# Kernel tuning notes

Measured on AMD Instinct MI355X. Metric: run time of the kernel, lower is better.

Reference implementation:

```python
import jax, jax.numpy as jnp
import numpy as np

SIDE = 64; EMB = 16; CH = 64; K = 64; V = 64; L = 8
N = SIDE * SIDE

def _pos_table(side, d):
    pe = np.array([[p / np.power(10000, 2 * (j // 2) / d) for j in range(d)]
                   if p != 0 else np.zeros(d) for p in range(side)])
    pe[1:, 0::2] = np.sin(pe[1:, 0::2])
    pe[1:, 1::2] = np.cos(pe[1:, 1::2])
    return pe.astype(np.float32)  # [side, d]

def _pos_emb():
    # Replicates torch .view(1, emb, side, 1): plain reshape of [side, emb] -> [emb, side]
    t = _pos_table(SIDE, EMB).reshape(EMB, SIDE)
    xe = np.broadcast_to(t[:, :, None], (EMB, SIDE, SIDE))
    ye = np.broadcast_to(t[:, None, :], (EMB, SIDE, SIDE))
    return jnp.asarray(np.concatenate([xe, ye], 0).reshape(1, 2 * EMB, N))

def _conv_mask():
    # CausalConv mask, see_center=False, 5x5: zero center pixel onward in center row, and all rows below
    m = np.ones((CH, 3, 5, 5), np.float32)
    m[:, :, 2, 2:] = 0.0
    m[:, :, 3:, :] = 0.0
    return jnp.asarray(m)

def _lrelu(x):
    return jnp.where(x >= 0, x, 0.01 * x)  # LeakyReLU(0.01)

def _bn(x, g, b, eps=1e-5):
    # training-mode batch norm (biased variance), channel axis = 1
    axes = (0,) + tuple(range(2, x.ndim))
    m = jnp.mean(x, axes, keepdims=True)
    var = jnp.mean((x - m) ** 2, axes, keepdims=True)
    sh = (1, -1) + (1,) * (x.ndim - 2)
    return g.reshape(sh) * (x - m) / jnp.sqrt(var + eps) + b.reshape(sh)

def _cv1(w, b, x):
    # 1x1 Conv1d: [O,I] x [B,I,N] -> [B,O,N]
    return jnp.einsum('oi,bin->bon', w, x) + b[:, None]

def reference(x, conv_w, conv_b, bn0_g, bn0_b, q_w, q_b, fk_w, fk_b, ck_w, ck_b,
              fv_w, fv_b, cv_w, cv_b, bn_g, bn_b, out_w, out_b):
    B = x.shape[0]
    pos = jnp.broadcast_to(_pos_emb(), (B, 2 * EMB, N))
    mask = jnp.tril(jnp.ones((N, N), jnp.float32))

    # masked causal conv input layer + BN + LeakyReLU
    w = conv_w * _conv_mask()
    h = jax.lax.conv_general_dilated(x, w, (1, 1), [(2, 2), (2, 2)],
                                     dimension_numbers=('NCHW', 'OIHW', 'NCHW'))
    h = h + conv_b[None, :, None, None]
    h = _lrelu(_bn(h, bn0_g, bn0_b)).reshape(B, CH, N)

    k0 = jnp.zeros((B, K, N), x.dtype)
    v0 = jnp.zeros((B, V, N), x.dtype)
    inv_sqrt_k = 1.0 / jnp.sqrt(jnp.float32(K))

    def layer(carry, p):
        h, k, v = carry
        qw, qb, fkw, fkb, ckw, ckb, fvw, fvb, cvw, cvb, g, bb = p
        x0 = jnp.concatenate([h, pos], 1)            # [B, CH+32, N]
        x0k = jnp.concatenate([x0, k], 1)            # [B, 160, N]
        x0v = jnp.concatenate([x0, v], 1)
        fk = jax.nn.sigmoid(_cv1(fkw, fkb, x0k))
        ck = _lrelu(_cv1(ckw, ckb, x0k))
        k_new = fk * k + ck                          # highway-gated persistent K
        fv = jax.nn.sigmoid(_cv1(fvw, fvb, x0v))
        cv_ = _lrelu(_cv1(cvw, cvb, x0v))
        v_new = fv * v + cv_
        q = _lrelu(_cv1(qw, qb, x0))                 # [B, K, N]
        attn = jnp.einsum('bkn,bkm->bnm', q, k) * inv_sqrt_k  # uses OLD k
        attn = attn * mask + (1.0 - mask) * (-10000.0)
        attn = jax.nn.softmax(attn, axis=-1) * mask
        out1 = jnp.einsum('bnm,bvm->bvn', attn, v)   # uses OLD v; [B, V, N]
        # original code computes fc(out1) but discards it (out2 overwritten)
        h2 = _lrelu(_bn(out1, g, bb))
        return (h2, k_new, v_new), None

    params = (q_w, q_b, fk_w, fk_b, ck_w, ck_b, fv_w, fv_b, cv_w, cv_b, bn_g, bn_b)
    (h, k, v), _ = jax.lax.scan(layer, (h, k0, v0), params)

    out = jnp.einsum('oi,bin->bon', out_w, h) + out_b[None, :, None]
    return out.reshape(B, out_w.shape[0], SIDE, SIDE)

def setup_inputs() -> dict:
    key = jax.random.key(0)
    ks = jax.random.split(key, 12)
    s = 0.05
    return {
        'x': jax.random.normal(ks[0], (2, 3, 64, 64), jnp.float32),
        'conv_w': jax.random.normal(ks[1], (CH, 3, 5, 5), jnp.float32) * s,
        'conv_b': jnp.zeros((CH,), jnp.float32),
        'bn0_g': jnp.ones((CH,), jnp.float32),
        'bn0_b': jnp.zeros((CH,), jnp.float32),
        'q_w': jax.random.normal(ks[2], (L, K, CH + 2 * EMB), jnp.float32) * s,
        'q_b': jnp.zeros((L, K), jnp.float32),
        'fk_w': jax.random.normal(ks[3], (L, K, CH + K + 2 * EMB), jnp.float32) * s,
        'fk_b': jnp.zeros((L, K), jnp.float32),
        'ck_w': jax.random.normal(ks[4], (L, K, CH + K + 2 * EMB), jnp.float32) * s,
        'ck_b': jnp.zeros((L, K), jnp.float32),
        'fv_w': jax.random.normal(ks[5], (L, V, CH + V + 2 * EMB), jnp.float32) * s,
        'fv_b': jnp.zeros((L, V), jnp.float32),
        'cv_w': jax.random.normal(ks[6], (L, V, CH + V + 2 * EMB), jnp.float32) * s,
        'cv_b': jnp.zeros((L, V), jnp.float32),
        'bn_g': jnp.ones((L, CH), jnp.float32),
        'bn_b': jnp.zeros((L, CH), jnp.float32),
        'out_w': jax.random.normal(ks[7], (100, V), jnp.float32) * s,
        'out_b': jnp.zeros((100,), jnp.float32),
    }
```

## Files before the change

### kernel.cpp

```cpp
#include <hip/hip_runtime.h>

#define NPIX 4096
#define CHN  64

typedef __attribute__((ext_vector_type(8))) short short8;
typedef __attribute__((ext_vector_type(8))) unsigned short ushort8;
typedef __attribute__((ext_vector_type(4))) unsigned short ushort4v;
typedef __attribute__((ext_vector_type(4))) float f32x4;
typedef __attribute__((ext_vector_type(16))) float f32x16;

__device__ __forceinline__ float lrelu_(float x){ return x >= 0.f ? x : 0.01f*x; }

__device__ __forceinline__ unsigned short f2bf(float x){
  union { float f; unsigned u; } v; v.f = x;
  unsigned r = v.u + 0x7FFF + ((v.u >> 16) & 1);
  return (unsigned short)(r >> 16);
}
__device__ __forceinline__ float bf2f(unsigned short h){
  union { unsigned u; float f; } v; v.u = ((unsigned)h) << 16;
  return v.f;
}
__device__ __forceinline__ float asf_(unsigned u){
  union { unsigned u; float f; } v; v.u = u; return v.f;
}

__global__ void pos_kernel(float* __restrict__ pos){
  int idx = blockIdx.x*256 + threadIdx.x;
  int c = idx >> 12;
  int n = idx & (NPIX-1);
  int bcoord = (c < 16) ? (n >> 6) : (n & 63);
  int a = (c < 16) ? c : (c - 16);
  int flat = a*64 + bcoord;
  int p = flat >> 4;
  int j = flat & 15;
  float val = 0.f;
  if (p != 0){
    float ex = (float)(j & ~1) * (1.f/16.f);
    float w = powf(10000.f, -ex);
    float ang = (float)p * w;
    val = (j & 1) ? cosf(ang) : sinf(ang);
  }
  pos[idx] = val;
}

__global__ void wtr_kernel(const float* __restrict__ qw, const float* __restrict__ fkw,
                           const float* __restrict__ ckw, const float* __restrict__ fvw,
                           const float* __restrict__ cvw, const float* __restrict__ convw,
                           float* __restrict__ wt){
  int idx = blockIdx.x*256 + threadIdx.x;
  if (idx >= 381632) return;
  if (idx < 49152){
    int l = idx / 6144, r = idx % 6144, i = r >> 6, o = r & 63;
    wt[idx] = qw[(l*64 + o)*96 + i];
  } else if (idx < 376832){
    int e = idx - 49152;
    int mat = e / 81920, r = e % 81920;
    int l = r / 10240, rr = r % 10240, i = rr >> 6, o = rr & 63;
    const float* src = (mat==0) ? fkw : (mat==1) ? ckw : (mat==2) ? fvw : cvw;
    wt[idx] = src[(l*64 + o)*160 + i];
  } else {
    int e = idx - 376832;
    int o = e & 63, tap = e >> 6;
    int ci = tap / 25, r = tap % 25;
    wt[idx] = convw[(o*3 + ci)*25 + r];
  }
}

__global__ __launch_bounds__(256) void conv_in_kernel(const float* __restrict__ x,
                                                      const float* __restrict__ cwt,
                                                      const float* __restrict__ cb,
                                                      float* __restrict__ out){
  int t = threadIdx.x;
  int o = t & 63;
  int sub = t >> 6;
  int bid = blockIdx.x;
  int b = bid >> 10;
  int n = ((bid & 1023) << 2) + sub;
  int y = n >> 6, xx = n & 63;
  float acc = cb[o];
  #pragma unroll
  for (int ci=0; ci<3; ++ci){
    const float* xp = x + ((b*3+ci)<<12);
    #pragma unroll
    for (int ky=0; ky<3; ++ky){
      int yy = y + ky - 2;
      if (yy < 0) continue;
      int nk = (ky==2) ? 2 : 5;
      #pragma unroll
      for (int kx=0; kx<5; ++kx){
        if (kx >= nk) break;
        int xc = xx + kx - 2;
        if (xc < 0 || xc > 63) continue;
        acc += xp[(yy<<6) + xc] * cwt[(ci*25 + ky*5 + kx)*64 + o];
      }
    }
  }
  out[(b*CHN+o)*NPIX + n] = acc;
}

__global__ __launch_bounds__(1024) void bn_stats_kernel(const float* __restrict__ xin,
                                                        float* __restrict__ stats){
  int c = blockIdx.x;
  int t = threadIdx.x;
  float s = 0.f, ss = 0.f;
  #pragma unroll
  for (int it=0; it<8; ++it){
    int idx = t + it*1024;
    float v = xin[(((idx>>12))*CHN + c)*NPIX + (idx & (NPIX-1))];
    s += v; ss += v*v;
  }
  #pragma unroll
  for (int o=1; o<64; o<<=1){ s += __shfl_xor(s,o); ss += __shfl_xor(ss,o); }
  __shared__ float ps[16], pq[16];
  if ((t & 63) == 0){ ps[t>>6] = s; pq[t>>6] = ss; }
  __syncthreads();
  if (t == 0){
    float S=0.f, Q=0.f;
    #pragma unroll
    for (int i=0;i<16;++i){ S += ps[i]; Q += pq[i]; }
    float mu = S*(1.f/8192.f);
    float var = Q*(1.f/8192.f) - mu*mu;
    var = fmaxf(var, 0.f);
    stats[c*2]   = mu;
    stats[c*2+1] = rsqrtf(var + 1e-5f);
  }
}

__global__ void bn_apply_kernel(const float* __restrict__ xin, const float* __restrict__ stats,
                                const float* __restrict__ g, const float* __restrict__ bb,
                                float* __restrict__ hout){
  int idx = blockIdx.x*256 + threadIdx.x;
  int e = idx << 2;
  int c = (e >> 12) & 63;
  float mu = stats[c*2], rstd = stats[c*2+1];
  float gain = g[c]*rstd;
  float beta = bb[c] - gain*mu;
  float4 v = *(const float4*)(xin + e);
  float4 r;
  r.x = lrelu_(gain*v.x + beta);
  r.y = lrelu_(gain*v.y + beta);
  r.z = lrelu_(gain*v.z + beta);
  r.w = lrelu_(gain*v.w + beta);
  *(float4*)(hout + e) = r;
}

__global__ __launch_bounds__(256) void bn_apply2_kernel(float* __restrict__ hbuf,
                                                        const float* __restrict__ psum,
                                                        const float* __restrict__ psq,
                                                        const float* __restrict__ g,
                                                        const float* __restrict__ bb){
  int bid = blockIdx.x;
  int ebase = bid << 10;
  int c = (ebase >> 12) & 63;
  int t = threadIdx.x;
  float s = psum[c*256 + t];
  float q = psq[c*256 + t];
  #pragma unroll
  for (int o=1; o<64; o<<=1){ s += __shfl_xor(s,o); q += __shfl_xor(q,o); }
  __shared__ float as[4], aq[4];
  if ((t & 63) == 0){ as[t>>6] = s; aq[t>>6] = q; }
  __syncthreads();
  float S = as[0]+as[1]+as[2]+as[3];
  float Q = aq[0]+aq[1]+aq[2]+aq[3];
  float mu = S*(1.f/8192.f);
  float var = fmaxf(Q*(1.f/8192.f) - mu*mu, 0.f);
  float rstd = rsqrtf(var + 1e-5f);
  float gain = g[c]*rstd;
  float beta = bb[c] - gain*mu;
  float4 v = *(const float4*)(hbuf + ebase + t*4);
  float4 r;
  r.x = lrelu_(gain*v.x + beta);
  r.y = lrelu_(gain*v.y + beta);
  r.z = lrelu_(gain*v.z + beta);
  r.w = lrelu_(gain*v.w + beta);
  *(float4*)(hbuf + ebase + t*4) = r;
}

__global__ __launch_bounds__(256) void cv1_kernel(
    const float* __restrict__ hbuf, const float* __restrict__ pos,
    const float* __restrict__ kold, const float* __restrict__ vold,
    const float* __restrict__ qwt,
    const float* __restrict__ fkwt, const float* __restrict__ ckwt,
    const float* __restrict__ fvwt, const float* __restrict__ cvwt,
    const float* __restrict__ qbi,  const float* __restrict__ fkb,
    const float* __restrict__ ckb,  const float* __restrict__ fvb,
    const float* __restrict__ cvb,
    unsigned short* __restrict__ qh, unsigned short* __restrict__ ql,
    float* __restrict__ knew, unsigned short* __restrict__ khn, unsigned short* __restrict__ kln,
    float* __restrict__ vnew, unsigned short* __restrict__ vhTn, unsigned short* __restrict__ vlTn)
{
  int t = threadIdx.x;
  int o  = t & 63;
  int wv = t >> 6;
  int b    = blockIdx.x >> 8;
  int tile = blockIdx.x & 255;
  int n0 = tile*16 + wv*4;

  const float* hb = hbuf + b*CHN*NPIX + n0;
  const float* kb = kold + b*CHN*NPIX + n0;
  const float* vb = vold + b*CHN*NPIX + n0;
  const float* pb = pos + n0;

  auto load4 = [&](const float* p, float* dst){
    float4 a = *(const float4*)p;
    dst[0]=a.x; dst[1]=a.y; dst[2]=a.z; dst[3]=a.w;
  };

  float x[4];
  long obase = (long)(b*CHN+o)*NPIX + n0;
  size_t nbase = ((size_t)b*NPIX + n0)*64 + o;

  {
    float aq[4];
    float bias = qbi[o];
    #pragma unroll
    for (int j=0;j<4;++j) aq[j]=bias;
    #pragma unroll 4
    for (int i=0;i<64;++i){
      load4(hb + i*NPIX, x);
      float w = qwt[i*64 + o];
      #pragma unroll
      for (int j=0;j<4;++j) aq[j] += w*x[j];
    }
    #pragma unroll 4
    for (int i=0;i<32;++i){
      load4(pb + i*NPIX, x);
      float w = qwt[(64+i)*64 + o];
      #pragma unroll
      for (int j=0;j<4;++j) aq[j] += w*x[j];
    }
    #pragma unroll
    for (int j=0;j<4;++j){
      float v = lrelu_(aq[j]) * 0.125f;
      unsigned short hb16 = f2bf(v);
      qh[nbase + (size_t)j*64] = hb16;
      ql[nbase + (size_t)j*64] = f2bf(v - bf2f(hb16));
    }
  }

  {
    float af[4], ac[4];
    float bf = fkb[o], bc = ckb[o];
    #pragma unroll
    for (int j=0;j<4;++j){ af[j]=bf; ac[j]=bc; }
    #pragma unroll 4
    for (int i=0;i<64;++i){
      load4(hb + i*NPIX, x);
      float wf = fkwt[i*64+o], wc = ckwt[i*64+o];
      #pragma unroll
      for (int j=0;j<4;++j){ af[j] += wf*x[j]; ac[j] += wc*x[j]; }
    }
    #pragma unroll 4
    for (int i=0;i<32;++i){
      load4(pb + i*NPIX, x);
      float wf = fkwt[(64+i)*64+o], wc = ckwt[(64+i)*64+o];
      #pragma unroll
      for (int j=0;j<4;++j){ af[j] += wf*x[j]; ac[j] += wc*x[j]; }
    }
    #pragma unroll 4
    for (int i=0;i<64;++i){
      load4(kb + i*NPIX, x);
      float wf = fkwt[(96+i)*64+o], wc = ckwt[(96+i)*64+o];
      #pragma unroll
      for (int j=0;j<4;++j){ af[j] += wf*x[j]; ac[j] += wc*x[j]; }
    }
    float kv[4];
    load4(kb + o*NPIX, kv);
    #pragma unroll
    for (int j=0;j<4;++j){
      float fk = 1.f/(1.f+__expf(-af[j]));
      float kn = fk*kv[j] + lrelu_(ac[j]);
      knew[obase+j] = kn;
      unsigned short hb16 = f2bf(kn);
      khn[nbase + (size_t)j*64] = hb16;
      kln[nbase + (size_t)j*64] = f2bf(kn - bf2f(hb16));
    }
  }

  {
    float af[4], ac[4];
    float bf = fvb[o], bc = cvb[o];
    #pragma unroll
    for (int j=0;j<4;++j){ af[j]=bf; ac[j]=bc; }
    #pragma unroll 4
    for (int i=0;i<64;++i){
      load4(hb + i*NPIX, x);
      float wf = fvwt[i*64+o], wc = cvwt[i*64+o];
      #pragma unroll
      for (int j=0;j<4;++j){ af[j] += wf*x[j]; ac[j] += wc*x[j]; }
    }
    #pragma unroll 4
    for (int i=0;i<32;++i){
      load4(pb + i*NPIX, x);
      float wf = fvwt[(64+i)*64+o], wc = cvwt[(64+i)*64+o];
      #pragma unroll
      for (int j=0;j<4;++j){ af[j] += wf*x[j]; ac[j] += wc*x[j]; }
    }
    #pragma unroll 4
    for (int i=0;i<64;++i){
      load4(vb + i*NPIX, x);
      float wf = fvwt[(96+i)*64+o], wc = cvwt[(96+i)*64+o];
      #pragma unroll
      for (int j=0;j<4;++j){ af[j] += wf*x[j]; ac[j] += wc*x[j]; }
    }
    float vv[4];
    load4(vb + o*NPIX, vv);
    ushort4v vph, vpl;
    #pragma unroll
    for (int j=0;j<4;++j){
      float fv = 1.f/(1.f+__expf(-af[j]));
      float vn = fv*vv[j] + lrelu_(ac[j]);
      vnew[obase+j] = vn;
      unsigned short hb16 = f2bf(vn);
      vph[j] = hb16;
      vpl[j] = f2bf(vn - bf2f(hb16));
    }
    *(ushort4v*)(vhTn + ((size_t)(b*CHN+o))*NPIX + n0) = vph;
    *(ushort4v*)(vlTn + ((size_t)(b*CHN+o))*NPIX + n0) = vpl;
  }
}

__global__ __launch_bounds__(256) void attn_mfma(
    const unsigned short* __restrict__ qhg, const unsigned short* __restrict__ qlg,
    const unsigned short* __restrict__ khg, const unsigned short* __restrict__ klg,
    const unsigned short* __restrict__ vhg, const unsigned short* __restrict__ vlg,
    float* __restrict__ part)
{
  int bid = 287 - (int)blockIdx.x;
  int b = 0, id = bid;
  if (id >= 144){ b = 1; id -= 144; }
  int pidx = bid;
  int rem = id, k = 0;
  while (rem >= 4*(k+1)){ rem -= 4*(k+1); ++k; }
  int rtg   = 4*k + rem/(k+1);
  int chunk = rem - (rem/(k+1))*(k+1);

  int C0  = chunk << 9;
  int end = min(C0 + 512, rtg*128 + 128);
  int nt  = (end - C0 + 63) >> 6;

  int t = threadIdx.x;
  int w = t >> 6;
  int l = t & 63;
  int q = l & 31;
  int hi = l >> 5;
  int qbase = rtg*128 + w*32;
  int n_g = qbase + q;
  int nmax_w = qbase + 31;

  __shared__ __align__(16) char KH[8192], KL[8192];
  __shared__ __align__(16) char VH[8192], VL[8192];
  __shared__ __align__(16) char PH[4][4096], PL[4][4096];

  const unsigned short* qhp = qhg + (size_t)b*NPIX*64;
  const unsigned short* qlp = qlg + (size_t)b*NPIX*64;
  const unsigned short* khp = khg + (size_t)b*NPIX*64;
  const unsigned short* klp = klg + (size_t)b*NPIX*64;
  const unsigned short* vhp = vhg + (size_t)b*CHN*NPIX;
  const unsigned short* vlp = vlg + (size_t)b*CHN*NPIX;

  short8 qhf[4], qlf[4];
  #pragma unroll
  for (int kc=0; kc<4; ++kc){
    qhf[kc] = *(const short8*)(qhp + (size_t)n_g*64 + kc*16 + hi*8);
    qlf[kc] = *(const short8*)(qlp + (size_t)n_g*64 + kc*16 + hi*8);
  }

  int srow[2], scc8[2], soff[2];
  #pragma unroll
  for (int p=0; p<2; ++p){
    int slot = t + (p<<8);
    int row = slot >> 3, cc = slot & 7;
    srow[p] = row; scc8[p] = cc*8;
    soff[p] = row*128 + ((cc ^ (row & 7)) << 4);
  }
  ushort8 rkh[2], rkl[2], rvh[2], rvl[2];
  auto issue = [&](int m0){
    #pragma unroll
    for (int p=0; p<2; ++p){
      rkh[p] = *(const ushort8*)(khp + (size_t)(m0+srow[p])*64 + scc8[p]);
      rkl[p] = *(const ushort8*)(klp + (size_t)(m0+srow[p])*64 + scc8[p]);
      rvh[p] = *(const ushort8*)(vhp + (size_t)srow[p]*NPIX + m0 + scc8[p]);
      rvl[p] = *(const ushort8*)(vlp + (size_t)srow[p]*NPIX + m0 + scc8[p]);
    }
  };

  f32x16 oacc0, oacc1;
  #pragma unroll
  for (int i=0; i<16; ++i){ oacc0[i]=0.f; oacc1[i]=0.f; }
  float m_run = -1e30f, l_run = 0.f;

  char* phw = PH[w];
  char* plw = PL[w];

  issue(C0);
  for (int ti=0; ti<nt; ++ti){
    int m0 = C0 + (ti<<6);
    __syncthreads();
    #pragma unroll
    for (int p=0; p<2; ++p){
      *(ushort8*)(KH + soff[p]) = rkh[p];
      *(ushort8*)(KL + soff[p]) = rkl[p];
      *(ushort8*)(VH + soff[p]) = rvh[p];
      *(ushort8*)(VL + soff[p]) = rvl[p];
    }
    __syncthreads();
    if (ti+1 < nt) issue(m0 + 64);

    if (m0 <= nmax_w){
      f32x16 sf0, sf1;
      #pragma unroll
      for (int i=0; i<16; ++i){ sf0[i]=0.f; sf1[i]=0.f; }
      #pragma unroll
      for (int kc=0; kc<4; ++kc){
        int off0 = q*128 + (((2*kc + hi) ^ (q & 7)) << 4);
        short8 ah0 = *(const short8*)(KH + off0);
        short8 al0 = *(const short8*)(KL + off0);
        short8 ah1 = *(const short8*)(KH + off0 + 4096);
        short8 al1 = *(const short8*)(KL + off0 + 4096);
        sf0 = __builtin_amdgcn_mfma_f32_32x32x16_bf16(ah0, qhf[kc], sf0, 0,0,0);
        sf1 = __builtin_amdgcn_mfma_f32_32x32x16_bf16(ah1, qhf[kc], sf1, 0,0,0);
        sf0 = __builtin_amdgcn_mfma_f32_32x32x16_bf16(al0, qhf[kc], sf0, 0,0,0);
        sf1 = __builtin_amdgcn_mfma_f32_32x32x16_bf16(al1, qhf[kc], sf1, 0,0,0);
        sf0 = __builtin_amdgcn_mfma_f32_32x32x16_bf16(ah0, qlf[kc], sf0, 0,0,0);
        sf1 = __builtin_amdgcn_mfma_f32_32x32x16_bf16(ah1, qlf[kc], sf1, 0,0,0);
      }
      float mx = -1e30f;
      #pragma unroll
      for (int r=0; r<16; ++r){
        int mg0 = m0 + (r&3) + 8*(r>>2) + 4*hi;
        float s0 = (mg0 <= n_g) ? sf0[r] : -1e30f;
        float s1 = (mg0 + 32 <= n_g) ? sf1[r] : -1e30f;
        sf0[r] = s0; sf1[r] = s1;
        mx = fmaxf(mx, fmaxf(s0, s1));
      }
      mx = fmaxf(mx, __shfl_xor(mx, 32));
      float m_new = fmaxf(m_run, mx);
      float alpha = __expf(m_run - m_new);
      float ps = 0.f;
      #pragma unroll
      for (int r=0; r<16; ++r){
        float e0 = __expf(sf0[r] - m_new);
        float e1 = __expf(sf1[r] - m_new);
        sf0[r] = e0; sf1[r] = e1;
        ps += e0 + e1;
      }
      ps += __shfl_xor(ps, 32);
      l_run = l_run*alpha + ps;
      m_run = m_new;

      #pragma unroll
      for (int mf=0; mf<2; ++mf){
        #pragma unroll
        for (int qd=0; qd<4; ++qd){
          float a0 = mf ? sf1[4*qd]   : sf0[4*qd];
          float a1 = mf ? sf1[4*qd+1] : sf0[4*qd+1];
          float a2 = mf ? sf1[4*qd+2] : sf0[4*qd+2];
          float a3 = mf ? sf1[4*qd+3] : sf0[4*qd+3];
          unsigned wh0, wh1;
          asm("v_cvt_pk_bf16_f32 %0, %1, %2" : "=v"(wh0) : "v"(a0), "v"(a1));
          asm("v_cvt_pk_bf16_f32 %0, %1, %2" : "=v"(wh1) : "v"(a2), "v"(a3));
          float l0 = a0 - asf_(wh0 << 16);
          float l1 = a1 - asf_(wh0 & 0xffff0000u);
          float l2 = a2 - asf_(wh1 << 16);
          float l3 = a3 - asf_(wh1 & 0xffff0000u);
          unsigned wl0, wl1;
          asm("v_cvt_pk_bf16_f32 %0, %1, %2" : "=v"(wl0) : "v"(l0), "v"(l1));
          asm("v_cvt_pk_bf16_f32 %0, %1, %2" : "=v"(wl1) : "v"(l2), "v"(l3));
          int mchunk = 4*mf + qd;
          int boff = q*128 + ((mchunk ^ (q & 7)) << 4) + (hi << 3);
          *(uint2*)(phw + boff) = make_uint2(wh0, wh1);
          *(uint2*)(plw + boff) = make_uint2(wl0, wl1);
        }
      }
      #pragma unroll
      for (int i=0; i<16; ++i){ oacc0[i] *= alpha; oacc1[i] *= alpha; }

      #pragma unroll
      for (int kc=0; kc<4; ++kc){
        int poff = q*128 + (((2*kc + hi) ^ (q & 7)) << 4);
        short8 pfh = *(const short8*)(phw + poff);
        short8 pfl = *(const short8*)(plw + poff);
        short8 vh0 = *(const short8*)(VH + poff);
        short8 vl0 = *(const short8*)(VL + poff);
        short8 vh1 = *(const short8*)(VH + poff + 4096);
        short8 vl1 = *(const short8*)(VL + poff + 4096);
        oacc0 = __builtin_amdgcn_mfma_f32_32x32x16_bf16(vh0, pfh, oacc0, 0,0,0);
        oacc1 = __builtin_amdgcn_mfma_f32_32x32x16_bf16(vh1, pfh, oacc1, 0,0,0);
        oacc0 = __builtin_amdgcn_mfma_f32_32x32x16_bf16(vl0, pfh, oacc0, 0,0,0);
        oacc1 = __builtin_amdgcn_mfma_f32_32x32x16_bf16(vl1, pfh, oacc1, 0,0,0);
        oacc0 = __builtin_amdgcn_mfma_f32_32x32x16_bf16(vh0, pfl, oacc0, 0,0,0);
        oacc1 = __builtin_amdgcn_mfma_f32_32x32x16_bf16(vh1, pfl, oacc1, 0,0,0);
      }
    }
  }

  float* pacc = part + (size_t)pidx * 8448;
  #pragma unroll
  for (int vf=0; vf<2; ++vf){
    #pragma unroll
    for (int qd=0; qd<4; ++qd){
      int vd = 32*vf + 8*qd + 4*hi;
      f32x4 vv;
      vv.x = vf ? oacc1[4*qd]   : oacc0[4*qd];
      vv.y = vf ? oacc1[4*qd+1] : oacc0[4*qd+1];
      vv.z = vf ? oacc1[4*qd+2] : oacc0[4*qd+2];
      vv.w = vf ? oacc1[4*qd+3] : oacc0[4*qd+3];
      *(f32x4*)(pacc + (size_t)(w*32 + q)*64 + vd) = vv;
    }
  }
  if (l < 32){
    pacc[8192 + (w*32 + l)*2]     = m_run;
    pacc[8192 + (w*32 + l)*2 + 1] = l_run;
  }
}

__global__ __launch_bounds__(256) void attn_combine(const float* __restrict__ part,
                                                    float* __restrict__ out1,
                                                    float* __restrict__ psum,
                                                    float* __restrict__ psq){
  int bid = blockIdx.x;
  int b = bid >> 7, rt = bid & 127;
  int rtg = rt >> 2;
  int k2 = rtg >> 2;
  int nch = k2 + 1;
  int base = b*144 + 2*k2*(k2+1) + (rtg & 3)*(k2+1);

  int t = threadIdx.x;
  int nl = t & 31, vq = t >> 5;
  int row128 = (rt & 3)*32 + nl;

  float M = -1e30f;
  #pragma unroll
  for (int c=0; c<8; ++c)
    if (c < nch) M = fmaxf(M, part[(size_t)(base+c)*8448 + 8192 + row128*2]);

  float L = 0.f;
  float val[8];
  #pragma unroll
  for (int jj=0; jj<8; ++jj) val[jj] = 0.f;
  #pragma unroll
  for (int c=0; c<8; ++c){
    if (c < nch){
      const float* pa = part + (size_t)(base+c)*8448;
      float wgt = __expf(pa[8192 + row128*2] - M);
      L += pa[8192 + row128*2 + 1] * wgt;
      #pragma unroll
      for (int jj=0; jj<8; ++jj) val[jj] += wgt * pa[row128*64 + vq*8 + jj];
    }
  }
  float invL = 1.f / L;
  float s[8], q[8];
  #pragma unroll
  for (int jj=0; jj<8; ++jj){
    float v = val[jj]*invL;
    out1[((size_t)b*CHN + vq*8 + jj)*NPIX + rt*32 + nl] = v;
    s[jj] = v; q[jj] = v*v;
  }
  #pragma unroll
  for (int o2=1; o2<32; o2<<=1){
    #pragma unroll
    for (int jj=0; jj<8; ++jj){
      s[jj] += __shfl_xor(s[jj], o2);
      q[jj] += __shfl_xor(q[jj], o2);
    }
  }
  if (nl == 0){
    #pragma unroll
    for (int jj=0; jj<8; ++jj){
      int c = vq*8 + jj;
      psum[c*256 + bid] = s[jj];
      psq [c*256 + bid] = q[jj];
    }
  }
}

__global__ __launch_bounds__(256) void final_kernel(const float* __restrict__ h,
                                                    const float* __restrict__ ow,
                                                    const float* __restrict__ ob,
                                                    float* __restrict__ out){
  int idx = blockIdx.x*256 + threadIdx.x;
  int b  = idx / 409600;
  int r  = idx - b*409600;
  int oc = r >> 12;
  int n  = r & (NPIX-1);
  const float* hp = h + (size_t)b*CHN*NPIX + n;
  const float* wp = ow + oc*64;
  float acc = ob[oc];
  #pragma unroll
  for (int v=0; v<64; ++v) acc += wp[v]*hp[(size_t)v*NPIX];
  out[idx] = acc;
}

extern "C" void kernel_launch(void* const* d_in, const int* in_sizes, int n_in,
                              void* d_out, int out_size, void* d_ws, size_t ws_size,
                              hipStream_t stream){
  const float* x     = (const float*)d_in[0];
  const float* convw = (const float*)d_in[1];
  const float* convb = (const float*)d_in[2];
  const float* bn0g  = (const float*)d_in[3];
  const float* bn0b  = (const float*)d_in[4];
  const float* qw    = (const float*)d_in[5];
  const float* qbias = (const float*)d_in[6];
  const float* fkw   = (const float*)d_in[7];
  const float* fkb   = (const float*)d_in[8];
  const float* ckw   = (const float*)d_in[9];
  const float* ckb   = (const float*)d_in[10];
  const float* fvw   = (const float*)d_in[11];
  const float* fvb   = (const float*)d_in[12];
  const float* cvw   = (const float*)d_in[13];
  const float* cvb   = (const float*)d_in[14];
  const float* bng   = (const float*)d_in[15];
  const float* bnb   = (const float*)d_in[16];
  const float* ow    = (const float*)d_in[17];
  const float* ob    = (const float*)d_in[18];

  const size_t TEN = (size_t)2*CHN*NPIX;
  const size_t BFU = TEN/2;
  float* ws   = (float*)d_ws;
  float* pos  = ws;
  float* h    = pos + 32*NPIX;
  float* k0   = h  + TEN;
  float* k1   = k0 + TEN;
  float* v0   = k1 + TEN;
  float* v1   = v0 + TEN;
  float* stats = v1 + TEN;
  float* psum = stats + 128;
  float* psq  = psum + 64*256;
  float* wt   = psq + 64*256;
  float* bfb  = wt + 381632;
  unsigned short* qh  = (unsigned short*)(bfb);
  unsigned short* ql  = (unsigned short*)(bfb + BFU);
  unsigned short* kh0 = (unsigned short*)(bfb + 2*BFU);
  unsigned short* kh1 = (unsigned short*)(bfb + 3*BFU);
  unsigned short* kl0 = (unsigned short*)(bfb + 4*BFU);
  unsigned short* kl1 = (unsigned short*)(bfb + 5*BFU);
  unsigned short* vh0 = (unsigned short*)(bfb + 6*BFU);
  unsigned short* vh1 = (unsigned short*)(bfb + 7*BFU);
  unsigned short* vl0 = (unsigned short*)(bfb + 8*BFU);
  unsigned short* vl1 = (unsigned short*)(bfb + 9*BFU);
  float* part = bfb + 10*BFU;

  hipMemsetAsync(k0, 0, TEN*sizeof(float), stream);
  hipMemsetAsync(v0, 0, TEN*sizeof(float), stream);
  hipMemsetAsync(kh0, 0, TEN*2, stream);
  hipMemsetAsync(kl0, 0, TEN*2, stream);
  hipMemsetAsync(vh0, 0, TEN*2, stream);
  hipMemsetAsync(vl0, 0, TEN*2, stream);

  pos_kernel<<<512,256,0,stream>>>(pos);
  wtr_kernel<<<1491,256,0,stream>>>(qw, fkw, ckw, fvw, cvw, convw, wt);
  conv_in_kernel<<<2048,256,0,stream>>>(x, wt + 376832, convb, h);
  bn_stats_kernel<<<64,1024,0,stream>>>(h, stats);
  bn_apply_kernel<<<512,256,0,stream>>>(h, stats, bn0g, bn0b, h);

  float* kfp[2] = {k0,k1};
  float* vfp[2] = {v0,v1};
  unsigned short* khb[2] = {kh0,kh1};
  unsigned short* klb[2] = {kl0,kl1};
  unsigned short* vhb[2] = {vh0,vh1};
  unsigned short* vlb[2] = {vl0,vl1};
  for (int l=0; l<8; ++l){
    float* kold = kfp[l&1]; float* knew = kfp[(l+1)&1];
    float* vold = vfp[l&1]; float* vnew = vfp[(l+1)&1];
    cv1_kernel<<<512,256,0,stream>>>(h, pos, kold, vold,
        wt + l*6144,
        wt + 49152 + l*10240,
        wt + 49152 + 81920 + l*10240,
        wt + 49152 + 2*81920 + l*10240,
        wt + 49152 + 3*81920 + l*10240,
        qbias + l*64, fkb + l*64, ckb + l*64, fvb + l*64, cvb + l*64,
        qh, ql,
        knew, khb[(l+1)&1], klb[(l+1)&1],
        vnew, vhb[(l+1)&1], vlb[(l+1)&1]);
    attn_mfma<<<288,256,0,stream>>>(qh, ql, khb[l&1], klb[l&1], vhb[l&1], vlb[l&1], part);
    attn_combine<<<256,256,0,stream>>>(part, h, psum, psq);
    bn_apply2_kernel<<<512,256,0,stream>>>(h, psum, psq, bng + l*64, bnb + l*64);
  }
  final_kernel<<<3200,256,0,stream>>>(h, ow, ob, (float*)d_out);
}
```

Measured before the change: 847.6 us.

## Halve attention block size and pass P fragments via lane shuffles, not LDS

Attention now runs 576 blocks of 128 threads, each owning 64 query rows instead of 128, so more blocks are in flight and causal work is balanced more finely. The combine kernel's partial indexing is updated to match. The softmax probabilities are packed to bf16 hi/lo in registers and rearranged into MFMA B-operand layout with cross-half-wave shuffles, removing the per-wave P scratch in shared memory and its write/read round trip. In exchange each K/V tile is loaded by half as many threads, so each tile is loaded by more blocks overall, and the shuffles plus selects add VALU work.

```diff
diff --git a/kernel.cpp b/kernel.cpp
--- a/kernel.cpp
+++ b/kernel.cpp
@@ -8,6 +8,7 @@
 typedef __attribute__((ext_vector_type(4))) unsigned short ushort4v;
 typedef __attribute__((ext_vector_type(4))) float f32x4;
 typedef __attribute__((ext_vector_type(16))) float f32x16;
+typedef __attribute__((ext_vector_type(4))) unsigned int uint4v;
 
 __device__ __forceinline__ float lrelu_(float x){ return x >= 0.f ? x : 0.01f*x; }
 
@@ -320,23 +321,41 @@
   }
 }
 
-__global__ __launch_bounds__(256) void attn_mfma(
+__device__ __forceinline__ void pack_sf(const f32x16& sfv, unsigned (&ph)[4][2],
+                                        unsigned (&pl)[4][2]){
+  #pragma unroll
+  for (int a=0; a<4; ++a){
+    unsigned h0, h1;
+    asm("v_cvt_pk_bf16_f32 %0, %1, %2" : "=v"(h0) : "v"(sfv[4*a]),   "v"(sfv[4*a+1]));
+    asm("v_cvt_pk_bf16_f32 %0, %1, %2" : "=v"(h1) : "v"(sfv[4*a+2]), "v"(sfv[4*a+3]));
+    float r0 = sfv[4*a]   - asf_(h0 << 16);
+    float r1 = sfv[4*a+1] - asf_(h0 & 0xffff0000u);
+    float r2 = sfv[4*a+2] - asf_(h1 << 16);
+    float r3 = sfv[4*a+3] - asf_(h1 & 0xffff0000u);
+    unsigned l0, l1;
+    asm("v_cvt_pk_bf16_f32 %0, %1, %2" : "=v"(l0) : "v"(r0), "v"(r1));
+    asm("v_cvt_pk_bf16_f32 %0, %1, %2" : "=v"(l1) : "v"(r2), "v"(r3));
+    ph[a][0]=h0; ph[a][1]=h1; pl[a][0]=l0; pl[a][1]=l1;
+  }
+}
+
+__global__ __launch_bounds__(128) void attn_mfma(
     const unsigned short* __restrict__ qhg, const unsigned short* __restrict__ qlg,
     const unsigned short* __restrict__ khg, const unsigned short* __restrict__ klg,
     const unsigned short* __restrict__ vhg, const unsigned short* __restrict__ vlg,
     float* __restrict__ part)
 {
-  int bid = 287 - (int)blockIdx.x;
+  int bid = 575 - (int)blockIdx.x;
   int b = 0, id = bid;
-  if (id >= 144){ b = 1; id -= 144; }
+  if (id >= 288){ b = 1; id -= 288; }
   int pidx = bid;
   int rem = id, k = 0;
-  while (rem >= 4*(k+1)){ rem -= 4*(k+1); ++k; }
-  int rtg   = 4*k + rem/(k+1);
+  while (rem >= 8*(k+1)){ rem -= 8*(k+1); ++k; }
+  int rt    = 8*k + rem/(k+1);
   int chunk = rem - (rem/(k+1))*(k+1);
 
   int C0  = chunk << 9;
-  int end = min(C0 + 512, rtg*128 + 128);
+  int end = min(C0 + 512, rt*64 + 64);
   int nt  = (end - C0 + 63) >> 6;
 
   int t = threadIdx.x;
@@ -344,13 +363,12 @@
   int l = t & 63;
   int q = l & 31;
   int hi = l >> 5;
-  int qbase = rtg*128 + w*32;
+  int qbase = rt*64 + w*32;
   int n_g = qbase + q;
   int nmax_w = qbase + 31;
 
   __shared__ __align__(16) char KH[8192], KL[8192];
   __shared__ __align__(16) char VH[8192], VL[8192];
-  __shared__ __align__(16) char PH[4][4096], PL[4][4096];
 
   const unsigned short* qhp = qhg + (size_t)b*NPIX*64;
   const unsigned short* qlp = qlg + (size_t)b*NPIX*64;
@@ -366,18 +384,18 @@
     qlf[kc] = *(const short8*)(qlp + (size_t)n_g*64 + kc*16 + hi*8);
   }
 
-  int srow[2], scc8[2], soff[2];
-  #pragma unroll
-  for (int p=0; p<2; ++p){
-    int slot = t + (p<<8);
+  int srow[4], scc8[4], soff[4];
+  #pragma unroll
+  for (int p=0; p<4; ++p){
+    int slot = t + (p<<7);
     int row = slot >> 3, cc = slot & 7;
     srow[p] = row; scc8[p] = cc*8;
     soff[p] = row*128 + ((cc ^ (row & 7)) << 4);
   }
-  ushort8 rkh[2], rkl[2], rvh[2], rvl[2];
+  ushort8 rkh[4], rkl[4], rvh[4], rvl[4];
   auto issue = [&](int m0){
     #pragma unroll
-    for (int p=0; p<2; ++p){
+    for (int p=0; p<4; ++p){
       rkh[p] = *(const ushort8*)(khp + (size_t)(m0+srow[p])*64 + scc8[p]);
       rkl[p] = *(const ushort8*)(klp + (size_t)(m0+srow[p])*64 + scc8[p]);
       rvh[p] = *(const ushort8*)(vhp + (size_t)srow[p]*NPIX + m0 + scc8[p]);
@@ -390,15 +408,12 @@
   for (int i=0; i<16; ++i){ oacc0[i]=0.f; oacc1[i]=0.f; }
   float m_run = -1e30f, l_run = 0.f;
 
-  char* phw = PH[w];
-  char* plw = PL[w];
-
   issue(C0);
   for (int ti=0; ti<nt; ++ti){
     int m0 = C0 + (ti<<6);
     __syncthreads();
     #pragma unroll
-    for (int p=0; p<2; ++p){
+    for (int p=0; p<4; ++p){
       *(ushort8*)(KH + soff[p]) = rkh[p];
       *(ushort8*)(KL + soff[p]) = rkl[p];
       *(ushort8*)(VH + soff[p]) = rvh[p];
@@ -449,53 +464,53 @@
       l_run = l_run*alpha + ps;
       m_run = m_new;
 
-      #pragma unroll
-      for (int mf=0; mf<2; ++mf){
-        #pragma unroll
-        for (int qd=0; qd<4; ++qd){
-          float a0 = mf ? sf1[4*qd]   : sf0[4*qd];
-          float a1 = mf ? sf1[4*qd+1] : sf0[4*qd+1];
-          float a2 = mf ? sf1[4*qd+2] : sf0[4*qd+2];
-          float a3 = mf ? sf1[4*qd+3] : sf0[4*qd+3];
-          unsigned wh0, wh1;
-          asm("v_cvt_pk_bf16_f32 %0, %1, %2" : "=v"(wh0) : "v"(a0), "v"(a1));
-          asm("v_cvt_pk_bf16_f32 %0, %1, %2" : "=v"(wh1) : "v"(a2), "v"(a3));
-          float l0 = a0 - asf_(wh0 << 16);
-          float l1 = a1 - asf_(wh0 & 0xffff0000u);
-          float l2 = a2 - asf_(wh1 << 16);
-          float l3 = a3 - asf_(wh1 & 0xffff0000u);
-          unsigned wl0, wl1;
-          asm("v_cvt_pk_bf16_f32 %0, %1, %2" : "=v"(wl0) : "v"(l0), "v"(l1));
-          asm("v_cvt_pk_bf16_f32 %0, %1, %2" : "=v"(wl1) : "v"(l2), "v"(l3));
-          int mchunk = 4*mf + qd;
-          int boff = q*128 + ((mchunk ^ (q & 7)) << 4) + (hi << 3);
-          *(uint2*)(phw + boff) = make_uint2(wh0, wh1);
-          *(uint2*)(plw + boff) = make_uint2(wl0, wl1);
-        }
-      }
+      unsigned ph0[4][2], pl0[4][2], ph1[4][2], pl1[4][2];
+      pack_sf(sf0, ph0, pl0);
+      pack_sf(sf1, ph1, pl1);
+
       #pragma unroll
       for (int i=0; i<16; ++i){ oacc0[i] *= alpha; oacc1[i] *= alpha; }
 
-      #pragma unroll
-      for (int kc=0; kc<4; ++kc){
-        int poff = q*128 + (((2*kc + hi) ^ (q & 7)) << 4);
-        short8 pfh = *(const short8*)(phw + poff);
-        short8 pfl = *(const short8*)(plw + poff);
-        short8 vh0 = *(const short8*)(VH + poff);
-        short8 vl0 = *(const short8*)(VL + poff);
-        short8 vh1 = *(const short8*)(VH + poff + 4096);
-        short8 vl1 = *(const short8*)(VL + poff + 4096);
-        oacc0 = __builtin_amdgcn_mfma_f32_32x32x16_bf16(vh0, pfh, oacc0, 0,0,0);
-        oacc1 = __builtin_amdgcn_mfma_f32_32x32x16_bf16(vh1, pfh, oacc1, 0,0,0);
-        oacc0 = __builtin_amdgcn_mfma_f32_32x32x16_bf16(vl0, pfh, oacc0, 0,0,0);
-        oacc1 = __builtin_amdgcn_mfma_f32_32x32x16_bf16(vl1, pfh, oacc1, 0,0,0);
-        oacc0 = __builtin_amdgcn_mfma_f32_32x32x16_bf16(vh0, pfl, oacc0, 0,0,0);
-        oacc1 = __builtin_amdgcn_mfma_f32_32x32x16_bf16(vh1, pfl, oacc1, 0,0,0);
-      }
-    }
-  }
-
-  float* pacc = part + (size_t)pidx * 8448;
+#define PV_KC(KC, PH, PL) { \
+      const int kk = (KC)&1; \
+      unsigned oh0 = hi ? PH[2*kk+1][0] : PH[2*kk][0]; \
+      unsigned oh1 = hi ? PH[2*kk+1][1] : PH[2*kk][1]; \
+      unsigned sh0 = hi ? PH[2*kk][0]   : PH[2*kk+1][0]; \
+      unsigned sh1 = hi ? PH[2*kk][1]   : PH[2*kk+1][1]; \
+      unsigned rh0 = __shfl_xor(sh0, 32); \
+      unsigned rh1 = __shfl_xor(sh1, 32); \
+      unsigned ol0 = hi ? PL[2*kk+1][0] : PL[2*kk][0]; \
+      unsigned ol1 = hi ? PL[2*kk+1][1] : PL[2*kk][1]; \
+      unsigned sl0 = hi ? PL[2*kk][0]   : PL[2*kk+1][0]; \
+      unsigned sl1 = hi ? PL[2*kk][1]   : PL[2*kk+1][1]; \
+      unsigned rl0 = __shfl_xor(sl0, 32); \
+      unsigned rl1 = __shfl_xor(sl1, 32); \
+      union { uint4v u; short8 s; } fh, fl; \
+      fh.u[0] = hi ? rh0 : oh0; fh.u[1] = hi ? rh1 : oh1; \
+      fh.u[2] = hi ? oh0 : rh0; fh.u[3] = hi ? oh1 : rh1; \
+      fl.u[0] = hi ? rl0 : ol0; fl.u[1] = hi ? rl1 : ol1; \
+      fl.u[2] = hi ? ol0 : rl0; fl.u[3] = hi ? ol1 : rl1; \
+      int poff = q*128 + (((2*(KC) + hi) ^ (q & 7)) << 4); \
+      short8 xvh0 = *(const short8*)(VH + poff); \
+      short8 xvl0 = *(const short8*)(VL + poff); \
+      short8 xvh1 = *(const short8*)(VH + poff + 4096); \
+      short8 xvl1 = *(const short8*)(VL + poff + 4096); \
+      oacc0 = __builtin_amdgcn_mfma_f32_32x32x16_bf16(xvh0, fh.s, oacc0, 0,0,0); \
+      oacc1 = __builtin_amdgcn_mfma_f32_32x32x16_bf16(xvh1, fh.s, oacc1, 0,0,0); \
+      oacc0 = __builtin_amdgcn_mfma_f32_32x32x16_bf16(xvl0, fh.s, oacc0, 0,0,0); \
+      oacc1 = __builtin_amdgcn_mfma_f32_32x32x16_bf16(xvl1, fh.s, oacc1, 0,0,0); \
+      oacc0 = __builtin_amdgcn_mfma_f32_32x32x16_bf16(xvh0, fl.s, oacc0, 0,0,0); \
+      oacc1 = __builtin_amdgcn_mfma_f32_32x32x16_bf16(xvh1, fl.s, oacc1, 0,0,0); \
+    }
+      PV_KC(0, ph0, pl0)
+      PV_KC(1, ph0, pl0)
+      PV_KC(2, ph1, pl1)
+      PV_KC(3, ph1, pl1)
+#undef PV_KC
+    }
+  }
+
+  float* pacc = part + (size_t)pidx * 4224;
   #pragma unroll
   for (int vf=0; vf<2; ++vf){
     #pragma unroll
@@ -510,8 +525,8 @@
     }
   }
   if (l < 32){
-    pacc[8192 + (w*32 + l)*2]     = m_run;
-    pacc[8192 + (w*32 + l)*2 + 1] = l_run;
+    pacc[4096 + (w*32 + l)*2]     = m_run;
+    pacc[4096 + (w*32 + l)*2 + 1] = l_run;
   }
 }
 
@@ -521,19 +536,19 @@
                                                     float* __restrict__ psq){
   int bid = blockIdx.x;
   int b = bid >> 7, rt = bid & 127;
-  int rtg = rt >> 2;
-  int k2 = rtg >> 2;
+  int rt64 = rt >> 1;
+  int k2 = rt64 >> 3;
   int nch = k2 + 1;
-  int base = b*144 + 2*k2*(k2+1) + (rtg & 3)*(k2+1);
+  int base = b*288 + 4*k2*(k2+1) + (rt64 - 8*k2)*nch;
 
   int t = threadIdx.x;
   int nl = t & 31, vq = t >> 5;
-  int row128 = (rt & 3)*32 + nl;
+  int row64 = (rt & 1)*32 + nl;
 
   float M = -1e30f;
   #pragma unroll
   for (int c=0; c<8; ++c)
-    if (c < nch) M = fmaxf(M, part[(size_t)(base+c)*8448 + 8192 + row128*2]);
+    if (c < nch) M = fmaxf(M, part[(size_t)(base+c)*4224 + 4096 + row64*2]);
 
   float L = 0.f;
   float val[8];
@@ -542,11 +557,11 @@
   #pragma unroll
   for (int c=0; c<8; ++c){
     if (c < nch){
-      const float* pa = part + (size_t)(base+c)*8448;
-      float wgt = __expf(pa[8192 + row128*2] - M);
-      L += pa[8192 + row128*2 + 1] * wgt;
-      #pragma unroll
-      for (int jj=0; jj<8; ++jj) val[jj] += wgt * pa[row128*64 + vq*8 + jj];
+      const float* pa = part + (size_t)(base+c)*4224;
+      float wgt = __expf(pa[4096 + row64*2] - M);
+      L += pa[4096 + row64*2 + 1] * wgt;
+      #pragma unroll
+      for (int jj=0; jj<8; ++jj) val[jj] += wgt * pa[row64*64 + vq*8 + jj];
     }
   }
   float invL = 1.f / L;
@@ -673,7 +688,7 @@
         qh, ql,
         knew, khb[(l+1)&1], klb[(l+1)&1],
         vnew, vhb[(l+1)&1], vlb[(l+1)&1]);
-    attn_mfma<<<288,256,0,stream>>>(qh, ql, khb[l&1], klb[l&1], vhb[l&1], vlb[l&1], part);
+    attn_mfma<<<576,128,0,stream>>>(qh, ql, khb[l&1], klb[l&1], vhb[l&1], vlb[l&1], part);
     attn_combine<<<256,256,0,stream>>>(part, h, psum, psq);
     bn_apply2_kernel<<<512,256,0,stream>>>(h, psum, psq, bng + l*64, bnb + l*64);
   }
```

Measured after the change: 857.7 us. Within noise of the previous version (+1.2%).
